# Optimization experiments

Measured on AMD Instinct MI355X. Metric: run time of the kernel, lower is better.

## Reference

```python
import jax, jax.numpy as jnp
import numpy as np

N = 1024    # num_points
HID = 1024  # Hamiltonian MLP hidden width


def setup_inputs() -> dict:
    key = jax.random.key(0)
    ks = jax.random.split(key, 6)
    def w(k, shape, fan_in):
        return jax.random.normal(k, shape, dtype=jnp.float32) / np.float32(np.sqrt(fan_in))
    return {
        "x": jax.random.normal(ks[0], (N,), dtype=jnp.float32),
        "q": jax.random.normal(ks[1], (N,), dtype=jnp.float32),
        "p": jax.random.normal(ks[2], (N,), dtype=jnp.float32),
        "W1": w(ks[3], (3 * N, HID), 3 * N),
        "b1": jnp.zeros((HID,), dtype=jnp.float32),
        "W2": w(ks[4], (HID, HID), HID),
        "b2": jnp.zeros((HID,), dtype=jnp.float32),
        "W3": w(ks[5], (HID, 1), HID),
        "b3": jnp.zeros((1,), dtype=jnp.float32),
    }


def _hamiltonian(z, W1, b1, W2, b2, W3, b3):
    # H: R^{3N} -> scalar (matches self.H(cat([x,q,p])).sum())
    h = jnp.tanh(z @ W1 + b1)
    h = jnp.tanh(h @ W2 + b2)
    return jnp.sum(h @ W3 + b3)


def reference(x, q, p, W1, b1, W2, b2, W3, b3):
    n = x.shape[0]

    def grads_qp(x_):
        # (dH/dq, dH/dp) as a function of x, with q,p closed over
        f = lambda q_, p_: _hamiltonian(jnp.concatenate([x_, q_, p_]), W1, b1, W2, b2, W3, b3)
        return jax.grad(f, argnums=(0, 1))(q, p)  # each [n]

    # Diagonal of cross-Hessian blocks via forward-over-reverse, batched over
    # all n basis directions at once (replaces the per-index autograd loop).
    eye = jnp.eye(n, dtype=x.dtype)

    def diag_entry(e_i, i):
        _, (dgq, dgp) = jax.jvp(grads_qp, (x,), (e_i,))
        return dgq[i], dgp[i]  # d2H/(dx_i dq_i), d2H/(dx_i dp_i)

    dH_dq_dx, dH_dp_dx = jax.vmap(diag_entry)(eye, jnp.arange(n))  # each [n]
    return dH_dp_dx, -dH_dq_dx
```

## Files before the change

### kernel.cpp

```cpp
#include <hip/hip_runtime.h>
#include <math.h>

typedef unsigned short u16;
typedef __bf16 bf16x8 __attribute__((ext_vector_type(8)));
typedef float f32x4 __attribute__((ext_vector_type(4)));

__device__ inline u16 bf16_rn(float x) {
    unsigned u = __float_as_uint(x);
    return (u16)((u + 0x7FFFu + ((u >> 16) & 1u)) >> 16);
}
__device__ inline void split2(float x, u16& h, u16& l) {
    h = bf16_rn(x);
    float hf = __uint_as_float(((unsigned)h) << 16);
    l = bf16_rn(x - hf);
}
__device__ inline uint2 pack4(u16 a, u16 b, u16 c, u16 d) {
    uint2 r;
    r.x = (unsigned)a | ((unsigned)b << 16);
    r.y = (unsigned)c | ((unsigned)d << 16);
    return r;
}
__device__ inline f32x4 mfma16(bf16x8 a, bf16x8 b, f32x4 c) {
    return __builtin_amdgcn_mfma_f32_16x16x32_bf16(a, b, c, 0, 0, 0);
}

__global__ __launch_bounds__(256) void k_pre(const float* __restrict__ x,
                                             const float* __restrict__ q,
                                             const float* __restrict__ p,
                                             const float* __restrict__ W1,
                                             u16* __restrict__ Ah, u16* __restrict__ Al,
                                             float* __restrict__ Upart,
                                             float* __restrict__ out,
                                             float* __restrict__ Vacc) {
    int b = blockIdx.x, t = threadIdx.x;
    if (b < 1024) {
        int idx = (b * 256 + t) * 4;
        float4 v = *(const float4*)(W1 + idx);
        u16 h0, l0, h1, l1, h2, l2, h3, l3;
        split2(v.x, h0, l0); split2(v.y, h1, l1); split2(v.z, h2, l2); split2(v.w, h3, l3);
        *(uint2*)&Ah[idx] = pack4(h0, h1, h2, h3);
        *(uint2*)&Al[idx] = pack4(l0, l1, l2, l3);
    } else if (b < 1216) {
        int jc = b - 1024;
        int k = (jc & 3) * 256 + t;
        int j0 = (jc >> 2) * 64;
        __shared__ float zs[64];
        if (t < 64) {
            int j = j0 + t;
            zs[t] = (j < 1024) ? x[j] : (j < 2048 ? q[j - 1024] : p[j - 2048]);
        }
        __syncthreads();
        float acc = 0.f;
#pragma unroll 8
        for (int j = 0; j < 64; ++j) acc += zs[j] * W1[(j0 + j) * 1024 + k];
        Upart[(jc >> 2) * 1024 + k] = acc;
    } else {
        int idx = ((b - 1216) * 256 + t) * 4;
        if (idx < 2048) *(float4*)(out + idx) = make_float4(0.f, 0.f, 0.f, 0.f);
        else *(float4*)(Vacc + idx - 2048) = make_float4(0.f, 0.f, 0.f, 0.f);
    }
}

__global__ __launch_bounds__(256) void k_w2v(const float* __restrict__ W2,
                                             const float* __restrict__ b1,
                                             const float* __restrict__ Upart,
                                             float* __restrict__ H1g, float* __restrict__ D1g,
                                             u16* __restrict__ W2h, u16* __restrict__ W2l,
                                             u16* __restrict__ WTh, u16* __restrict__ WTl,
                                             float* __restrict__ Vacc) {
    __shared__ float T[64][65];
    __shared__ float hs[64], ds[64];
    int k0 = blockIdx.y * 64, m0 = blockIdx.x * 64;
    int t = threadIdx.x;
    if (t < 64) {
        float u = 0.f;
#pragma unroll 8
        for (int c = 0; c < 48; ++c) u += Upart[c * 1024 + k0 + t];
        float h = tanhf(u + b1[k0 + t]);
        hs[t] = h;
        ds[t] = 1.f - h * h;
        if (m0 == 0) { H1g[k0 + t] = h; D1g[k0 + t] = 1.f - h * h; }
    }
    __syncthreads();
    int rr = t >> 4, cc = (t & 15) * 4;
    float4 vp = make_float4(0.f, 0.f, 0.f, 0.f);
#pragma unroll
    for (int j = 0; j < 4; ++j) {
        int r = rr + j * 16;
        float4 v = *(const float4*)(W2 + (k0 + r) * 1024 + m0 + cc);
        T[r][cc + 0] = v.x; T[r][cc + 1] = v.y; T[r][cc + 2] = v.z; T[r][cc + 3] = v.w;
        u16 h0, l0, h1, l1, h2, l2, h3, l3;
        split2(v.x, h0, l0); split2(v.y, h1, l1); split2(v.z, h2, l2); split2(v.w, h3, l3);
        *(uint2*)&W2h[(k0 + r) * 1024 + m0 + cc] = pack4(h0, h1, h2, h3);
        *(uint2*)&W2l[(k0 + r) * 1024 + m0 + cc] = pack4(l0, l1, l2, l3);
        float hk = hs[r];
        vp.x += hk * v.x; vp.y += hk * v.y; vp.z += hk * v.z; vp.w += hk * v.w;
    }
    vp.x += __shfl_xor(vp.x, 16); vp.y += __shfl_xor(vp.y, 16);
    vp.z += __shfl_xor(vp.z, 16); vp.w += __shfl_xor(vp.w, 16);
    vp.x += __shfl_xor(vp.x, 32); vp.y += __shfl_xor(vp.y, 32);
    vp.z += __shfl_xor(vp.z, 32); vp.w += __shfl_xor(vp.w, 32);
    if (((t & 63) >> 4) == 0) {
        atomicAdd(&Vacc[m0 + cc + 0], vp.x);
        atomicAdd(&Vacc[m0 + cc + 1], vp.y);
        atomicAdd(&Vacc[m0 + cc + 2], vp.z);
        atomicAdd(&Vacc[m0 + cc + 3], vp.w);
    }
    __syncthreads();
#pragma unroll
    for (int j = 0; j < 4; ++j) {
        int mrow = rr + j * 16;
        float f0 = T[cc + 0][mrow] * ds[cc + 0];
        float f1 = T[cc + 1][mrow] * ds[cc + 1];
        float f2 = T[cc + 2][mrow] * ds[cc + 2];
        float f3 = T[cc + 3][mrow] * ds[cc + 3];
        u16 h0, l0, h1, l1, h2, l2, h3, l3;
        split2(f0, h0, l0); split2(f1, h1, l1); split2(f2, h2, l2); split2(f3, h3, l3);
        *(uint2*)&WTh[(m0 + mrow) * 1024 + k0 + cc] = pack4(h0, h1, h2, h3);
        *(uint2*)&WTl[(m0 + mrow) * 1024 + k0 + cc] = pack4(l0, l1, l2, l3);
    }
}

__global__ __launch_bounds__(256) void k_g(const float* __restrict__ W2,
                                           const float* __restrict__ Vacc,
                                           const float* __restrict__ b2,
                                           const float* __restrict__ W3,
                                           const float* __restrict__ H1,
                                           const float* __restrict__ D1,
                                           float* __restrict__ Avec) {
    __shared__ float sv[1024];
    int k = blockIdx.x;
    int t = threadIdx.x;
#pragma unroll
    for (int j = 0; j < 4; ++j) {
        int m = t * 4 + j;
        float h = tanhf(Vacc[m] + b2[m]);
        sv[m] = (1.f - h * h) * W3[m];
    }
    __syncthreads();
    float acc = 0.f;
#pragma unroll
    for (int m = t; m < 1024; m += 256) acc += W2[k * 1024 + m] * sv[m];
    for (int o = 32; o; o >>= 1) acc += __shfl_down(acc, o);
    __shared__ float red[4];
    int lane = t & 63, w = t >> 6;
    if (lane == 0) red[w] = acc;
    __syncthreads();
    if (t == 0) Avec[k] = -2.f * H1[k] * D1[k] * (red[0] + red[1] + red[2] + red[3]);
}

#define LDK 68
__global__ __launch_bounds__(256) void k_gemm1(const u16* __restrict__ Ah, const u16* __restrict__ Al,
                                               const u16* __restrict__ Bh, const u16* __restrict__ Bl,
                                               const float* __restrict__ Vacc,
                                               const float* __restrict__ b2,
                                               const float* __restrict__ W3,
                                               u16* __restrict__ Sh, u16* __restrict__ Sl) {
    __shared__ u16 As[2][2][64 * LDK];
    __shared__ u16 Bs[2][2][64 * LDK];
    int tid = threadIdx.x, lane = tid & 63, wv = tid >> 6;
    int wy = wv >> 1, wx = wv & 1;
    int i0 = blockIdx.y * 64, m0 = blockIdx.x * 64;
    int srow = tid >> 2, sseg = (tid & 3) * 16;
    int ldso = srow * LDK + sseg;
    const u16* ap_h = Ah + (i0 + srow) * 1024 + sseg;
    const u16* ap_l = Al + (i0 + srow) * 1024 + sseg;
    const u16* bp_h = Bh + (m0 + srow) * 1024 + sseg;
    const u16* bp_l = Bl + (m0 + srow) * 1024 + sseg;
    int tx = lane & 15, qy = lane >> 4;
    int raA0 = (wy * 32 + tx) * LDK, raA1 = raA0 + 16 * LDK;
    int rbB0 = (wx * 32 + tx) * LDK, rbB1 = rbB0 + 16 * LDK;
    f32x4 acc[2][2];
#pragma unroll
    for (int a = 0; a < 2; ++a)
#pragma unroll
        for (int b = 0; b < 2; ++b) acc[a][b] = (f32x4){0.f, 0.f, 0.f, 0.f};

    *(uint4*)&As[0][0][ldso] = *(const uint4*)(ap_h);
    *(uint4*)&As[0][0][ldso + 8] = *(const uint4*)(ap_h + 8);
    *(uint4*)&As[0][1][ldso] = *(const uint4*)(ap_l);
    *(uint4*)&As[0][1][ldso + 8] = *(const uint4*)(ap_l + 8);
    *(uint4*)&Bs[0][0][ldso] = *(const uint4*)(bp_h);
    *(uint4*)&Bs[0][0][ldso + 8] = *(const uint4*)(bp_h + 8);
    *(uint4*)&Bs[0][1][ldso] = *(const uint4*)(bp_l);
    *(uint4*)&Bs[0][1][ldso + 8] = *(const uint4*)(bp_l + 8);

    for (int k0 = 0; k0 < 1024; k0 += 64) {
        int buf = (k0 >> 6) & 1;
        int kn = (k0 + 64) & 1023;
        uint4 pa0 = *(const uint4*)(ap_h + kn), pa1 = *(const uint4*)(ap_h + kn + 8);
        uint4 pb0 = *(const uint4*)(ap_l + kn), pb1 = *(const uint4*)(ap_l + kn + 8);
        uint4 pc0 = *(const uint4*)(bp_h + kn), pc1 = *(const uint4*)(bp_h + kn + 8);
        uint4 pd0 = *(const uint4*)(bp_l + kn), pd1 = *(const uint4*)(bp_l + kn + 8);
        __syncthreads();
#pragma unroll
        for (int ks = 0; ks < 2; ++ks) {
            int o = ks * 32 + qy * 8;
            bf16x8 aH0 = *(const bf16x8*)&As[buf][0][raA0 + o];
            bf16x8 aH1 = *(const bf16x8*)&As[buf][0][raA1 + o];
            bf16x8 aL0 = *(const bf16x8*)&As[buf][1][raA0 + o];
            bf16x8 aL1 = *(const bf16x8*)&As[buf][1][raA1 + o];
            bf16x8 bH0 = *(const bf16x8*)&Bs[buf][0][rbB0 + o];
            bf16x8 bH1 = *(const bf16x8*)&Bs[buf][0][rbB1 + o];
            bf16x8 bL0 = *(const bf16x8*)&Bs[buf][1][rbB0 + o];
            bf16x8 bL1 = *(const bf16x8*)&Bs[buf][1][rbB1 + o];
            acc[0][0] = mfma16(aH0, bH0, acc[0][0]);
            acc[0][0] = mfma16(aH0, bL0, acc[0][0]);
            acc[0][0] = mfma16(aL0, bH0, acc[0][0]);
            acc[0][1] = mfma16(aH0, bH1, acc[0][1]);
            acc[0][1] = mfma16(aH0, bL1, acc[0][1]);
            acc[0][1] = mfma16(aL0, bH1, acc[0][1]);
            acc[1][0] = mfma16(aH1, bH0, acc[1][0]);
            acc[1][0] = mfma16(aH1, bL0, acc[1][0]);
            acc[1][0] = mfma16(aL1, bH0, acc[1][0]);
            acc[1][1] = mfma16(aH1, bH1, acc[1][1]);
            acc[1][1] = mfma16(aH1, bL1, acc[1][1]);
            acc[1][1] = mfma16(aL1, bH1, acc[1][1]);
        }
        int nb = buf ^ 1;
        *(uint4*)&As[nb][0][ldso] = pa0; *(uint4*)&As[nb][0][ldso + 8] = pa1;
        *(uint4*)&As[nb][1][ldso] = pb0; *(uint4*)&As[nb][1][ldso + 8] = pb1;
        *(uint4*)&Bs[nb][0][ldso] = pc0; *(uint4*)&Bs[nb][0][ldso + 8] = pc1;
        *(uint4*)&Bs[nb][1][ldso] = pd0; *(uint4*)&Bs[nb][1][ldso + 8] = pd1;
    }
#pragma unroll
    for (int sj = 0; sj < 2; ++sj) {
        int m = m0 + wx * 32 + sj * 16 + tx;
        float hv = tanhf(Vacc[m] + b2[m]);
        float d2 = 1.f - hv * hv;
        float cm = -2.f * hv * d2 * W3[m];
#pragma unroll
        for (int si = 0; si < 2; ++si) {
            int ib = i0 + wy * 32 + si * 16 + qy * 4;
#pragma unroll
            for (int r = 0; r < 4; ++r) {
                float v = acc[si][sj][r] * cm;
                u16 h, l;
                split2(v, h, l);
                Sh[(ib + r) * 1024 + m] = h;
                Sl[(ib + r) * 1024 + m] = l;
            }
        }
    }
}

__global__ __launch_bounds__(256) void k_gemm2(const u16* __restrict__ Sh, const u16* __restrict__ Sl,
                                               const u16* __restrict__ W2h, const u16* __restrict__ W2l,
                                               const float* __restrict__ W1,
                                               const float* __restrict__ D1,
                                               const float* __restrict__ Avec,
                                               float* __restrict__ out) {
    __shared__ u16 As[2][2][64 * LDK];
    __shared__ u16 Bs[2][2][64 * LDK];
    int tid = threadIdx.x, lane = tid & 63, wv = tid >> 6;
    int wy = wv >> 1, wx = wv & 1;
    int i0 = blockIdx.y * 64, k0g = blockIdx.x * 64;
    int srow = tid >> 2, sseg = (tid & 3) * 16;
    int ldso = srow * LDK + sseg;
    const u16* ap_h = Sh + (i0 + srow) * 1024 + sseg;
    const u16* ap_l = Sl + (i0 + srow) * 1024 + sseg;
    const u16* bp_h = W2h + (k0g + srow) * 1024 + sseg;
    const u16* bp_l = W2l + (k0g + srow) * 1024 + sseg;
    int tx = lane & 15, qy = lane >> 4;
    int raA0 = (wy * 32 + tx) * LDK, raA1 = raA0 + 16 * LDK;
    int rbB0 = (wx * 32 + tx) * LDK, rbB1 = rbB0 + 16 * LDK;
    f32x4 acc[2][2];
#pragma unroll
    for (int a = 0; a < 2; ++a)
#pragma unroll
        for (int b = 0; b < 2; ++b) acc[a][b] = (f32x4){0.f, 0.f, 0.f, 0.f};

    *(uint4*)&As[0][0][ldso] = *(const uint4*)(ap_h);
    *(uint4*)&As[0][0][ldso + 8] = *(const uint4*)(ap_h + 8);
    *(uint4*)&As[0][1][ldso] = *(const uint4*)(ap_l);
    *(uint4*)&As[0][1][ldso + 8] = *(const uint4*)(ap_l + 8);
    *(uint4*)&Bs[0][0][ldso] = *(const uint4*)(bp_h);
    *(uint4*)&Bs[0][0][ldso + 8] = *(const uint4*)(bp_h + 8);
    *(uint4*)&Bs[0][1][ldso] = *(const uint4*)(bp_l);
    *(uint4*)&Bs[0][1][ldso + 8] = *(const uint4*)(bp_l + 8);

    for (int m0 = 0; m0 < 1024; m0 += 64) {
        int buf = (m0 >> 6) & 1;
        int mn = (m0 + 64) & 1023;
        uint4 pa0 = *(const uint4*)(ap_h + mn), pa1 = *(const uint4*)(ap_h + mn + 8);
        uint4 pb0 = *(const uint4*)(ap_l + mn), pb1 = *(const uint4*)(ap_l + mn + 8);
        uint4 pc0 = *(const uint4*)(bp_h + mn), pc1 = *(const uint4*)(bp_h + mn + 8);
        uint4 pd0 = *(const uint4*)(bp_l + mn), pd1 = *(const uint4*)(bp_l + mn + 8);
        __syncthreads();
#pragma unroll
        for (int ks = 0; ks < 2; ++ks) {
            int o = ks * 32 + qy * 8;
            bf16x8 aH0 = *(const bf16x8*)&As[buf][0][raA0 + o];
            bf16x8 aH1 = *(const bf16x8*)&As[buf][0][raA1 + o];
            bf16x8 aL0 = *(const bf16x8*)&As[buf][1][raA0 + o];
            bf16x8 aL1 = *(const bf16x8*)&As[buf][1][raA1 + o];
            bf16x8 bH0 = *(const bf16x8*)&Bs[buf][0][rbB0 + o];
            bf16x8 bH1 = *(const bf16x8*)&Bs[buf][0][rbB1 + o];
            bf16x8 bL0 = *(const bf16x8*)&Bs[buf][1][rbB0 + o];
            bf16x8 bL1 = *(const bf16x8*)&Bs[buf][1][rbB1 + o];
            acc[0][0] = mfma16(aH0, bH0, acc[0][0]);
            acc[0][0] = mfma16(aH0, bL0, acc[0][0]);
            acc[0][0] = mfma16(aL0, bH0, acc[0][0]);
            acc[0][1] = mfma16(aH0, bH1, acc[0][1]);
            acc[0][1] = mfma16(aH0, bL1, acc[0][1]);
            acc[0][1] = mfma16(aL0, bH1, acc[0][1]);
            acc[1][0] = mfma16(aH1, bH0, acc[1][0]);
            acc[1][0] = mfma16(aH1, bL0, acc[1][0]);
            acc[1][0] = mfma16(aL1, bH0, acc[1][0]);
            acc[1][1] = mfma16(aH1, bH1, acc[1][1]);
            acc[1][1] = mfma16(aH1, bL1, acc[1][1]);
            acc[1][1] = mfma16(aL1, bH1, acc[1][1]);
        }
        int nb = buf ^ 1;
        *(uint4*)&As[nb][0][ldso] = pa0; *(uint4*)&As[nb][0][ldso + 8] = pa1;
        *(uint4*)&As[nb][1][ldso] = pb0; *(uint4*)&As[nb][1][ldso + 8] = pb1;
        *(uint4*)&Bs[nb][0][ldso] = pc0; *(uint4*)&Bs[nb][0][ldso + 8] = pc1;
        *(uint4*)&Bs[nb][1][ldso] = pd0; *(uint4*)&Bs[nb][1][ldso + 8] = pd1;
    }
    int kk[2];
    float d1v[2], avv[2];
#pragma unroll
    for (int sj = 0; sj < 2; ++sj) {
        kk[sj] = k0g + wx * 32 + sj * 16 + tx;
        d1v[sj] = D1[kk[sj]];
        avv[sj] = Avec[kk[sj]];
    }
#pragma unroll
    for (int si = 0; si < 2; ++si) {
        int ib = i0 + wy * 32 + si * 16 + qy * 4;
#pragma unroll
        for (int r = 0; r < 4; ++r) {
            int i = ib + r;
            float pq = 0.f, pp = 0.f;
#pragma unroll
            for (int sj = 0; sj < 2; ++sj) {
                int k = kk[sj];
                float dr = avv[sj] * W1[i * 1024 + k] + d1v[sj] * acc[si][sj][r];
                pq += W1[(1024 + i) * 1024 + k] * dr;
                pp += W1[(2048 + i) * 1024 + k] * dr;
            }
            for (int o = 1; o < 16; o <<= 1) {
                pq += __shfl_xor(pq, o);
                pp += __shfl_xor(pp, o);
            }
            if (tx == 0) {
                atomicAdd(&out[i], pp);
                atomicAdd(&out[1024 + i], -pq);
            }
        }
    }
}

extern "C" void kernel_launch(void* const* d_in, const int* in_sizes, int n_in,
                              void* d_out, int out_size, void* d_ws, size_t ws_size,
                              hipStream_t stream) {
    const float* x = (const float*)d_in[0];
    const float* q = (const float*)d_in[1];
    const float* p = (const float*)d_in[2];
    const float* W1 = (const float*)d_in[3];
    const float* b1 = (const float*)d_in[4];
    const float* W2 = (const float*)d_in[5];
    const float* b2 = (const float*)d_in[6];
    const float* W3 = (const float*)d_in[7];
    float* out = (float*)d_out;
    float* ws = (float*)d_ws;
    float* H1 = ws, *D1 = ws + 1024, *Avec = ws + 2048, *Vacc = ws + 3072;
    float* Upart = ws + 4096;
    u16* u0 = (u16*)(ws + 65536);
    u16* Ah = u0;
    u16* Al = u0 + 1048576;
    u16* WTh = u0 + 2097152;
    u16* WTl = u0 + 3145728;
    u16* W2h = u0 + 4194304;
    u16* W2l = u0 + 5242880;
    u16* Sh = u0 + 6291456;
    u16* Sl = u0 + 7340032;

    k_pre<<<1219, 256, 0, stream>>>(x, q, p, W1, Ah, Al, Upart, out, Vacc);
    k_w2v<<<dim3(16, 16), 256, 0, stream>>>(W2, b1, Upart, H1, D1, W2h, W2l, WTh, WTl, Vacc);
    k_gemm1<<<dim3(16, 16), 256, 0, stream>>>(Ah, Al, WTh, WTl, Vacc, b2, W3, Sh, Sl);
    k_g<<<1024, 256, 0, stream>>>(W2, Vacc, b2, W3, H1, D1, Avec);
    k_gemm2<<<dim3(16, 16), 256, 0, stream>>>(Sh, Sl, W2h, W2l, W1, D1, Avec, out);
}
```

Before: 131.5 us.

## Split K across two wave groups in both GEMM kernels with LDS reduction

Both split-bf16 GEMM kernels now launch 512 threads per block. The extra four waves take the second 32-wide K half of each 64-wide tile, and their partial accumulators are merged through shared memory before the epilogue. The aim is more waves per CU to hide latency, since the grid is only 256 blocks on a large GPU. The cost is an extra LDS round-trip and barrier at the end, and half the waves sit idle during the epilogue.

```diff
diff --git a/kernel.cpp b/kernel.cpp
--- a/kernel.cpp
+++ b/kernel.cpp
@@ -150,7 +150,7 @@
 }
 
 #define LDK 68
-__global__ __launch_bounds__(256) void k_gemm1(const u16* __restrict__ Ah, const u16* __restrict__ Al,
+__global__ __launch_bounds__(512) void k_gemm1(const u16* __restrict__ Ah, const u16* __restrict__ Al,
                                                const u16* __restrict__ Bh, const u16* __restrict__ Bl,
                                                const float* __restrict__ Vacc,
                                                const float* __restrict__ b2,
@@ -159,17 +159,21 @@
     __shared__ u16 As[2][2][64 * LDK];
     __shared__ u16 Bs[2][2][64 * LDK];
     int tid = threadIdx.x, lane = tid & 63, wv = tid >> 6;
-    int wy = wv >> 1, wx = wv & 1;
+    int kh = wv >> 2, wy = (wv >> 1) & 1, wx = wv & 1;
     int i0 = blockIdx.y * 64, m0 = blockIdx.x * 64;
-    int srow = tid >> 2, sseg = (tid & 3) * 16;
+    int srow = tid >> 3, sseg = (tid & 7) * 8;
     int ldso = srow * LDK + sseg;
     const u16* ap_h = Ah + (i0 + srow) * 1024 + sseg;
     const u16* ap_l = Al + (i0 + srow) * 1024 + sseg;
     const u16* bp_h = Bh + (m0 + srow) * 1024 + sseg;
     const u16* bp_l = Bl + (m0 + srow) * 1024 + sseg;
     int tx = lane & 15, qy = lane >> 4;
-    int raA0 = (wy * 32 + tx) * LDK, raA1 = raA0 + 16 * LDK;
-    int rbB0 = (wx * 32 + tx) * LDK, rbB1 = rbB0 + 16 * LDK;
+    int koff = kh * 32 + qy * 8;
+    int raA[2], rbB[2];
+    raA[0] = (wy * 32 + tx) * LDK + koff;
+    raA[1] = raA[0] + 16 * LDK;
+    rbB[0] = (wx * 32 + tx) * LDK + koff;
+    rbB[1] = rbB[0] + 16 * LDK;
     f32x4 acc[2][2];
 #pragma unroll
     for (int a = 0; a < 2; ++a)
@@ -177,74 +181,86 @@
         for (int b = 0; b < 2; ++b) acc[a][b] = (f32x4){0.f, 0.f, 0.f, 0.f};
 
     *(uint4*)&As[0][0][ldso] = *(const uint4*)(ap_h);
-    *(uint4*)&As[0][0][ldso + 8] = *(const uint4*)(ap_h + 8);
     *(uint4*)&As[0][1][ldso] = *(const uint4*)(ap_l);
-    *(uint4*)&As[0][1][ldso + 8] = *(const uint4*)(ap_l + 8);
     *(uint4*)&Bs[0][0][ldso] = *(const uint4*)(bp_h);
-    *(uint4*)&Bs[0][0][ldso + 8] = *(const uint4*)(bp_h + 8);
     *(uint4*)&Bs[0][1][ldso] = *(const uint4*)(bp_l);
-    *(uint4*)&Bs[0][1][ldso + 8] = *(const uint4*)(bp_l + 8);
 
     for (int k0 = 0; k0 < 1024; k0 += 64) {
         int buf = (k0 >> 6) & 1;
         int kn = (k0 + 64) & 1023;
-        uint4 pa0 = *(const uint4*)(ap_h + kn), pa1 = *(const uint4*)(ap_h + kn + 8);
-        uint4 pb0 = *(const uint4*)(ap_l + kn), pb1 = *(const uint4*)(ap_l + kn + 8);
-        uint4 pc0 = *(const uint4*)(bp_h + kn), pc1 = *(const uint4*)(bp_h + kn + 8);
-        uint4 pd0 = *(const uint4*)(bp_l + kn), pd1 = *(const uint4*)(bp_l + kn + 8);
+        uint4 pa = *(const uint4*)(ap_h + kn);
+        uint4 pb = *(const uint4*)(ap_l + kn);
+        uint4 pc = *(const uint4*)(bp_h + kn);
+        uint4 pd = *(const uint4*)(bp_l + kn);
         __syncthreads();
-#pragma unroll
-        for (int ks = 0; ks < 2; ++ks) {
-            int o = ks * 32 + qy * 8;
-            bf16x8 aH0 = *(const bf16x8*)&As[buf][0][raA0 + o];
-            bf16x8 aH1 = *(const bf16x8*)&As[buf][0][raA1 + o];
-            bf16x8 aL0 = *(const bf16x8*)&As[buf][1][raA0 + o];
-            bf16x8 aL1 = *(const bf16x8*)&As[buf][1][raA1 + o];
-            bf16x8 bH0 = *(const bf16x8*)&Bs[buf][0][rbB0 + o];
-            bf16x8 bH1 = *(const bf16x8*)&Bs[buf][0][rbB1 + o];
-            bf16x8 bL0 = *(const bf16x8*)&Bs[buf][1][rbB0 + o];
-            bf16x8 bL1 = *(const bf16x8*)&Bs[buf][1][rbB1 + o];
-            acc[0][0] = mfma16(aH0, bH0, acc[0][0]);
-            acc[0][0] = mfma16(aH0, bL0, acc[0][0]);
-            acc[0][0] = mfma16(aL0, bH0, acc[0][0]);
-            acc[0][1] = mfma16(aH0, bH1, acc[0][1]);
-            acc[0][1] = mfma16(aH0, bL1, acc[0][1]);
-            acc[0][1] = mfma16(aL0, bH1, acc[0][1]);
-            acc[1][0] = mfma16(aH1, bH0, acc[1][0]);
-            acc[1][0] = mfma16(aH1, bL0, acc[1][0]);
-            acc[1][0] = mfma16(aL1, bH0, acc[1][0]);
-            acc[1][1] = mfma16(aH1, bH1, acc[1][1]);
-            acc[1][1] = mfma16(aH1, bL1, acc[1][1]);
-            acc[1][1] = mfma16(aL1, bH1, acc[1][1]);
-        }
+        bf16x8 aH0 = *(const bf16x8*)&As[buf][0][raA[0]];
+        bf16x8 aH1 = *(const bf16x8*)&As[buf][0][raA[1]];
+        bf16x8 aL0 = *(const bf16x8*)&As[buf][1][raA[0]];
+        bf16x8 aL1 = *(const bf16x8*)&As[buf][1][raA[1]];
+        bf16x8 bH0 = *(const bf16x8*)&Bs[buf][0][rbB[0]];
+        bf16x8 bH1 = *(const bf16x8*)&Bs[buf][0][rbB[1]];
+        bf16x8 bL0 = *(const bf16x8*)&Bs[buf][1][rbB[0]];
+        bf16x8 bL1 = *(const bf16x8*)&Bs[buf][1][rbB[1]];
+        acc[0][0] = mfma16(aH0, bH0, acc[0][0]);
+        acc[0][0] = mfma16(aH0, bL0, acc[0][0]);
+        acc[0][0] = mfma16(aL0, bH0, acc[0][0]);
+        acc[0][1] = mfma16(aH0, bH1, acc[0][1]);
+        acc[0][1] = mfma16(aH0, bL1, acc[0][1]);
+        acc[0][1] = mfma16(aL0, bH1, acc[0][1]);
+        acc[1][0] = mfma16(aH1, bH0, acc[1][0]);
+        acc[1][0] = mfma16(aH1, bL0, acc[1][0]);
+        acc[1][0] = mfma16(aL1, bH0, acc[1][0]);
+        acc[1][1] = mfma16(aH1, bH1, acc[1][1]);
+        acc[1][1] = mfma16(aH1, bL1, acc[1][1]);
+        acc[1][1] = mfma16(aL1, bH1, acc[1][1]);
         int nb = buf ^ 1;
-        *(uint4*)&As[nb][0][ldso] = pa0; *(uint4*)&As[nb][0][ldso + 8] = pa1;
-        *(uint4*)&As[nb][1][ldso] = pb0; *(uint4*)&As[nb][1][ldso + 8] = pb1;
-        *(uint4*)&Bs[nb][0][ldso] = pc0; *(uint4*)&Bs[nb][0][ldso + 8] = pc1;
-        *(uint4*)&Bs[nb][1][ldso] = pd0; *(uint4*)&Bs[nb][1][ldso + 8] = pd1;
-    }
-#pragma unroll
-    for (int sj = 0; sj < 2; ++sj) {
-        int m = m0 + wx * 32 + sj * 16 + tx;
-        float hv = tanhf(Vacc[m] + b2[m]);
-        float d2 = 1.f - hv * hv;
-        float cm = -2.f * hv * d2 * W3[m];
-#pragma unroll
-        for (int si = 0; si < 2; ++si) {
-            int ib = i0 + wy * 32 + si * 16 + qy * 4;
-#pragma unroll
-            for (int r = 0; r < 4; ++r) {
-                float v = acc[si][sj][r] * cm;
-                u16 h, l;
-                split2(v, h, l);
-                Sh[(ib + r) * 1024 + m] = h;
-                Sl[(ib + r) * 1024 + m] = l;
+        *(uint4*)&As[nb][0][ldso] = pa;
+        *(uint4*)&As[nb][1][ldso] = pb;
+        *(uint4*)&Bs[nb][0][ldso] = pc;
+        *(uint4*)&Bs[nb][1][ldso] = pd;
+    }
+    __syncthreads();
+    f32x4* mrg = (f32x4*)&As[0][0][0];
+    if (kh == 1) {
+#pragma unroll
+        for (int si = 0; si < 2; ++si)
+#pragma unroll
+            for (int sj = 0; sj < 2; ++sj)
+                mrg[(((wy * 2 + wx) * 4 + si * 2 + sj) * 4 + qy) * 16 + tx] = acc[si][sj];
+    }
+    __syncthreads();
+    if (kh == 0) {
+#pragma unroll
+        for (int si = 0; si < 2; ++si)
+#pragma unroll
+            for (int sj = 0; sj < 2; ++sj) {
+                f32x4 o = mrg[(((wy * 2 + wx) * 4 + si * 2 + sj) * 4 + qy) * 16 + tx];
+                acc[si][sj][0] += o[0]; acc[si][sj][1] += o[1];
+                acc[si][sj][2] += o[2]; acc[si][sj][3] += o[3];
+            }
+#pragma unroll
+        for (int sj = 0; sj < 2; ++sj) {
+            int m = m0 + wx * 32 + sj * 16 + tx;
+            float hv = tanhf(Vacc[m] + b2[m]);
+            float d2 = 1.f - hv * hv;
+            float cm = -2.f * hv * d2 * W3[m];
+#pragma unroll
+            for (int si = 0; si < 2; ++si) {
+                int ib = i0 + wy * 32 + si * 16 + qy * 4;
+#pragma unroll
+                for (int r = 0; r < 4; ++r) {
+                    float v = acc[si][sj][r] * cm;
+                    u16 h, l;
+                    split2(v, h, l);
+                    Sh[(ib + r) * 1024 + m] = h;
+                    Sl[(ib + r) * 1024 + m] = l;
+                }
             }
         }
     }
 }
 
-__global__ __launch_bounds__(256) void k_gemm2(const u16* __restrict__ Sh, const u16* __restrict__ Sl,
+__global__ __launch_bounds__(512) void k_gemm2(const u16* __restrict__ Sh, const u16* __restrict__ Sl,
                                                const u16* __restrict__ W2h, const u16* __restrict__ W2l,
                                                const float* __restrict__ W1,
                                                const float* __restrict__ D1,
@@ -253,17 +269,21 @@
     __shared__ u16 As[2][2][64 * LDK];
     __shared__ u16 Bs[2][2][64 * LDK];
     int tid = threadIdx.x, lane = tid & 63, wv = tid >> 6;
-    int wy = wv >> 1, wx = wv & 1;
+    int kh = wv >> 2, wy = (wv >> 1) & 1, wx = wv & 1;
     int i0 = blockIdx.y * 64, k0g = blockIdx.x * 64;
-    int srow = tid >> 2, sseg = (tid & 3) * 16;
+    int srow = tid >> 3, sseg = (tid & 7) * 8;
     int ldso = srow * LDK + sseg;
     const u16* ap_h = Sh + (i0 + srow) * 1024 + sseg;
     const u16* ap_l = Sl + (i0 + srow) * 1024 + sseg;
     const u16* bp_h = W2h + (k0g + srow) * 1024 + sseg;
     const u16* bp_l = W2l + (k0g + srow) * 1024 + sseg;
     int tx = lane & 15, qy = lane >> 4;
-    int raA0 = (wy * 32 + tx) * LDK, raA1 = raA0 + 16 * LDK;
-    int rbB0 = (wx * 32 + tx) * LDK, rbB1 = rbB0 + 16 * LDK;
+    int koff = kh * 32 + qy * 8;
+    int raA[2], rbB[2];
+    raA[0] = (wy * 32 + tx) * LDK + koff;
+    raA[1] = raA[0] + 16 * LDK;
+    rbB[0] = (wx * 32 + tx) * LDK + koff;
+    rbB[1] = rbB[0] + 16 * LDK;
     f32x4 acc[2][2];
 #pragma unroll
     for (int a = 0; a < 2; ++a)
@@ -271,81 +291,93 @@
         for (int b = 0; b < 2; ++b) acc[a][b] = (f32x4){0.f, 0.f, 0.f, 0.f};
 
     *(uint4*)&As[0][0][ldso] = *(const uint4*)(ap_h);
-    *(uint4*)&As[0][0][ldso + 8] = *(const uint4*)(ap_h + 8);
     *(uint4*)&As[0][1][ldso] = *(const uint4*)(ap_l);
-    *(uint4*)&As[0][1][ldso + 8] = *(const uint4*)(ap_l + 8);
     *(uint4*)&Bs[0][0][ldso] = *(const uint4*)(bp_h);
-    *(uint4*)&Bs[0][0][ldso + 8] = *(const uint4*)(bp_h + 8);
     *(uint4*)&Bs[0][1][ldso] = *(const uint4*)(bp_l);
-    *(uint4*)&Bs[0][1][ldso + 8] = *(const uint4*)(bp_l + 8);
 
     for (int m0 = 0; m0 < 1024; m0 += 64) {
         int buf = (m0 >> 6) & 1;
         int mn = (m0 + 64) & 1023;
-        uint4 pa0 = *(const uint4*)(ap_h + mn), pa1 = *(const uint4*)(ap_h + mn + 8);
-        uint4 pb0 = *(const uint4*)(ap_l + mn), pb1 = *(const uint4*)(ap_l + mn + 8);
-        uint4 pc0 = *(const uint4*)(bp_h + mn), pc1 = *(const uint4*)(bp_h + mn + 8);
-        uint4 pd0 = *(const uint4*)(bp_l + mn), pd1 = *(const uint4*)(bp_l + mn + 8);
+        uint4 pa = *(const uint4*)(ap_h + mn);
+        uint4 pb = *(const uint4*)(ap_l + mn);
+        uint4 pc = *(const uint4*)(bp_h + mn);
+        uint4 pd = *(const uint4*)(bp_l + mn);
         __syncthreads();
-#pragma unroll
-        for (int ks = 0; ks < 2; ++ks) {
-            int o = ks * 32 + qy * 8;
-            bf16x8 aH0 = *(const bf16x8*)&As[buf][0][raA0 + o];
-            bf16x8 aH1 = *(const bf16x8*)&As[buf][0][raA1 + o];
-            bf16x8 aL0 = *(const bf16x8*)&As[buf][1][raA0 + o];
-            bf16x8 aL1 = *(const bf16x8*)&As[buf][1][raA1 + o];
-            bf16x8 bH0 = *(const bf16x8*)&Bs[buf][0][rbB0 + o];
-            bf16x8 bH1 = *(const bf16x8*)&Bs[buf][0][rbB1 + o];
-            bf16x8 bL0 = *(const bf16x8*)&Bs[buf][1][rbB0 + o];
-            bf16x8 bL1 = *(const bf16x8*)&Bs[buf][1][rbB1 + o];
-            acc[0][0] = mfma16(aH0, bH0, acc[0][0]);
-            acc[0][0] = mfma16(aH0, bL0, acc[0][0]);
-            acc[0][0] = mfma16(aL0, bH0, acc[0][0]);
-            acc[0][1] = mfma16(aH0, bH1, acc[0][1]);
-            acc[0][1] = mfma16(aH0, bL1, acc[0][1]);
-            acc[0][1] = mfma16(aL0, bH1, acc[0][1]);
-            acc[1][0] = mfma16(aH1, bH0, acc[1][0]);
-            acc[1][0] = mfma16(aH1, bL0, acc[1][0]);
-            acc[1][0] = mfma16(aL1, bH0, acc[1][0]);
-            acc[1][1] = mfma16(aH1, bH1, acc[1][1]);
-            acc[1][1] = mfma16(aH1, bL1, acc[1][1]);
-            acc[1][1] = mfma16(aL1, bH1, acc[1][1]);
+        bf16x8 aH0 = *(const bf16x8*)&As[buf][0][raA[0]];
+        bf16x8 aH1 = *(const bf16x8*)&As[buf][0][raA[1]];
+        bf16x8 aL0 = *(const bf16x8*)&As[buf][1][raA[0]];
+        bf16x8 aL1 = *(const bf16x8*)&As[buf][1][raA[1]];
+        bf16x8 bH0 = *(const bf16x8*)&Bs[buf][0][rbB[0]];
+        bf16x8 bH1 = *(const bf16x8*)&Bs[buf][0][rbB[1]];
+        bf16x8 bL0 = *(const bf16x8*)&Bs[buf][1][rbB[0]];
+        bf16x8 bL1 = *(const bf16x8*)&Bs[buf][1][rbB[1]];
+        acc[0][0] = mfma16(aH0, bH0, acc[0][0]);
+        acc[0][0] = mfma16(aH0, bL0, acc[0][0]);
+        acc[0][0] = mfma16(aL0, bH0, acc[0][0]);
+        acc[0][1] = mfma16(aH0, bH1, acc[0][1]);
+        acc[0][1] = mfma16(aH0, bL1, acc[0][1]);
+        acc[0][1] = mfma16(aL0, bH1, acc[0][1]);
+        acc[1][0] = mfma16(aH1, bH0, acc[1][0]);
+        acc[1][0] = mfma16(aH1, bL0, acc[1][0]);
+        acc[1][0] = mfma16(aL1, bH0, acc[1][0]);
+        acc[1][1] = mfma16(aH1, bH1, acc[1][1]);
+        acc[1][1] = mfma16(aH1, bL1, acc[1][1]);
+        acc[1][1] = mfma16(aL1, bH1, acc[1][1]);
+        int nb = buf ^ 1;
+        *(uint4*)&As[nb][0][ldso] = pa;
+        *(uint4*)&As[nb][1][ldso] = pb;
+        *(uint4*)&Bs[nb][0][ldso] = pc;
+        *(uint4*)&Bs[nb][1][ldso] = pd;
+    }
+    __syncthreads();
+    f32x4* mrg = (f32x4*)&As[0][0][0];
+    if (kh == 1) {
+#pragma unroll
+        for (int si = 0; si < 2; ++si)
+#pragma unroll
+            for (int sj = 0; sj < 2; ++sj)
+                mrg[(((wy * 2 + wx) * 4 + si * 2 + sj) * 4 + qy) * 16 + tx] = acc[si][sj];
+    }
+    __syncthreads();
+    if (kh == 0) {
+#pragma unroll
+        for (int si = 0; si < 2; ++si)
+#pragma unroll
+            for (int sj = 0; sj < 2; ++sj) {
+                f32x4 o = mrg[(((wy * 2 + wx) * 4 + si * 2 + sj) * 4 + qy) * 16 + tx];
+                acc[si][sj][0] += o[0]; acc[si][sj][1] += o[1];
+                acc[si][sj][2] += o[2]; acc[si][sj][3] += o[3];
+            }
+        int kk[2];
+        float d1v[2], avv[2];
+#pragma unroll
+        for (int sj = 0; sj < 2; ++sj) {
+            kk[sj] = k0g + wx * 32 + sj * 16 + tx;
+            d1v[sj] = D1[kk[sj]];
+            avv[sj] = Avec[kk[sj]];
         }
-        int nb = buf ^ 1;
-        *(uint4*)&As[nb][0][ldso] = pa0; *(uint4*)&As[nb][0][ldso + 8] = pa1;
-        *(uint4*)&As[nb][1][ldso] = pb0; *(uint4*)&As[nb][1][ldso + 8] = pb1;
-        *(uint4*)&Bs[nb][0][ldso] = pc0; *(uint4*)&Bs[nb][0][ldso + 8] = pc1;
-        *(uint4*)&Bs[nb][1][ldso] = pd0; *(uint4*)&Bs[nb][1][ldso + 8] = pd1;
-    }
-    int kk[2];
-    float d1v[2], avv[2];
-#pragma unroll
-    for (int sj = 0; sj < 2; ++sj) {
-        kk[sj] = k0g + wx * 32 + sj * 16 + tx;
-        d1v[sj] = D1[kk[sj]];
-        avv[sj] = Avec[kk[sj]];
-    }
-#pragma unroll
-    for (int si = 0; si < 2; ++si) {
-        int ib = i0 + wy * 32 + si * 16 + qy * 4;
-#pragma unroll
-        for (int r = 0; r < 4; ++r) {
-            int i = ib + r;
-            float pq = 0.f, pp = 0.f;
-#pragma unroll
-            for (int sj = 0; sj < 2; ++sj) {
-                int k = kk[sj];
-                float dr = avv[sj] * W1[i * 1024 + k] + d1v[sj] * acc[si][sj][r];
-                pq += W1[(1024 + i) * 1024 + k] * dr;
-                pp += W1[(2048 + i) * 1024 + k] * dr;
-            }
-            for (int o = 1; o < 16; o <<= 1) {
-                pq += __shfl_xor(pq, o);
-                pp += __shfl_xor(pp, o);
-            }
-            if (tx == 0) {
-                atomicAdd(&out[i], pp);
-                atomicAdd(&out[1024 + i], -pq);
+#pragma unroll
+        for (int si = 0; si < 2; ++si) {
+            int ib = i0 + wy * 32 + si * 16 + qy * 4;
+#pragma unroll
+            for (int r = 0; r < 4; ++r) {
+                int i = ib + r;
+                float pq = 0.f, pp = 0.f;
+#pragma unroll
+                for (int sj = 0; sj < 2; ++sj) {
+                    int k = kk[sj];
+                    float dr = avv[sj] * W1[i * 1024 + k] + d1v[sj] * acc[si][sj][r];
+                    pq += W1[(1024 + i) * 1024 + k] * dr;
+                    pp += W1[(2048 + i) * 1024 + k] * dr;
+                }
+                for (int o = 1; o < 16; o <<= 1) {
+                    pq += __shfl_xor(pq, o);
+                    pp += __shfl_xor(pp, o);
+                }
+                if (tx == 0) {
+                    atomicAdd(&out[i], pp);
+                    atomicAdd(&out[1024 + i], -pq);
+                }
             }
         }
     }
@@ -378,7 +410,7 @@
 
     k_pre<<<1219, 256, 0, stream>>>(x, q, p, W1, Ah, Al, Upart, out, Vacc);
     k_w2v<<<dim3(16, 16), 256, 0, stream>>>(W2, b1, Upart, H1, D1, W2h, W2l, WTh, WTl, Vacc);
-    k_gemm1<<<dim3(16, 16), 256, 0, stream>>>(Ah, Al, WTh, WTl, Vacc, b2, W3, Sh, Sl);
+    k_gemm1<<<dim3(16, 16), 512, 0, stream>>>(Ah, Al, WTh, WTl, Vacc, b2, W3, Sh, Sl);
     k_g<<<1024, 256, 0, stream>>>(W2, Vacc, b2, W3, H1, D1, Avec);
-    k_gemm2<<<dim3(16, 16), 256, 0, stream>>>(Sh, Sl, W2h, W2l, W1, D1, Avec, out);
-}
+    k_gemm2<<<dim3(16, 16), 512, 0, stream>>>(Sh, Sl, W2h, W2l, W1, D1, Avec, out);
+}
```

New measurement: 127.8 us. 2.9% less time.
